# Kernel optimization log

Measured on AMD Instinct MI355X. Metric: run time of the kernel, lower is better.

## Reference

```python
import jax, jax.numpy as jnp
import numpy as np

H = 768            # hidden_size
IMG_H = 1024       # image_hidden_size
NH = 12            # num_heads
NKV = 1            # num_kv_heads (MQA)
HD = H // NH       # head_dim = 64
FF = 4 * H         # intermediate_size = 3072
EPS = 1e-5


def layernorm(x, g, b):
    m = jnp.mean(x, axis=-1, keepdims=True)
    v = jnp.mean(jnp.square(x - m), axis=-1, keepdims=True)
    return (x - m) * jax.lax.rsqrt(v + EPS) * g + b


def setup_inputs() -> dict:
    key = jax.random.key(0)
    ks = jax.random.split(key, 12)
    B, NQ, NIMG = 8, 256, 4096
    s = 0.02
    return {
        "hidden_states": jax.random.normal(ks[0], (B, NQ, H), jnp.float32),
        "image_features": jax.random.normal(ks[1], (B, NIMG, IMG_H), jnp.float32),
        # norm_image_pre
        "ln_img_g": jnp.ones((IMG_H,), jnp.float32),
        "ln_img_b": jnp.zeros((IMG_H,), jnp.float32),
        # image_bottleneck (bias=False)
        "W_bottle": jax.random.normal(ks[2], (IMG_H, H), jnp.float32) * s,
        # norm_hidden
        "ln_h_g": jnp.ones((H,), jnp.float32),
        "ln_h_b": jnp.zeros((H,), jnp.float32),
        # to_q
        "Wq": jax.random.normal(ks[3], (H, H), jnp.float32) * s,
        "bq": jnp.zeros((H,), jnp.float32),
        # to_kv: out = num_kv_heads * head_dim * 2
        "Wkv": jax.random.normal(ks[4], (H, 2 * NKV * HD), jnp.float32) * s,
        "bkv": jnp.zeros((2 * NKV * HD,), jnp.float32),
        # to_out
        "Wo": jax.random.normal(ks[5], (H, H), jnp.float32) * s,
        "bo": jnp.zeros((H,), jnp.float32),
        # attn_out_norm
        "ln_ao_g": jnp.ones((H,), jnp.float32),
        "ln_ao_b": jnp.zeros((H,), jnp.float32),
        # gate
        "gate_param": jnp.zeros((), jnp.float32),
        # ffn_norm
        "ln_f_g": jnp.ones((H,), jnp.float32),
        "ln_f_b": jnp.zeros((H,), jnp.float32),
        # ffn
        "W1": jax.random.normal(ks[6], (H, FF), jnp.float32) * s,
        "b1": jnp.zeros((FF,), jnp.float32),
        "W2": jax.random.normal(ks[7], (FF, H), jnp.float32) * s,
        "b2": jnp.zeros((H,), jnp.float32),
    }


def reference(hidden_states, image_features, ln_img_g, ln_img_b, W_bottle,
              ln_h_g, ln_h_b, Wq, bq, Wkv, bkv, Wo, bo, ln_ao_g, ln_ao_b,
              gate_param, ln_f_g, ln_f_b, W1, b1, W2, b2):
    B, NQ, _ = hidden_states.shape
    # image pre-norm + bottleneck
    img = layernorm(image_features, ln_img_g, ln_img_b)
    img = img @ W_bottle                                   # [B, Nimg, H]
    # query path
    q_in = layernorm(hidden_states, ln_h_g, ln_h_b)
    q = (q_in @ Wq + bq).reshape(B, NQ, NH, HD).transpose(0, 2, 1, 3)  # b h i d
    # kv path (MQA: single shared KV head)
    kv = (img @ Wkv + bkv).reshape(B, -1, 2, NKV, HD)
    k = kv[:, :, 0, 0, :]                                  # [B, Nimg, HD]
    v = kv[:, :, 1, 0, :]
    scale = 1.0 / np.sqrt(HD)
    # broadcast KV across heads instead of explicit repeat
    scores = jnp.einsum('bhid,bjd->bhij', q * scale, k)    # [B, NH, NQ, Nimg]
    attn = jax.nn.softmax(scores, axis=-1)                 # dropout is identity (eval)
    out = jnp.einsum('bhij,bjd->bhid', attn, v)
    out = out.transpose(0, 2, 1, 3).reshape(B, NQ, H)
    out = out @ Wo + bo
    out = layernorm(out, ln_ao_g, ln_ao_b)
    gate = jax.nn.sigmoid(gate_param)
    h = hidden_states + gate * out
    ffn_in = layernorm(h, ln_f_g, ln_f_b)
    ffn_out = jax.nn.gelu(ffn_in @ W1 + b1, approximate=False) @ W2 + b2
    return h + ffn_out
```

## Files before the change

### kernel.cpp

```cpp
#include <hip/hip_runtime.h>
#include <cstdint>

typedef unsigned short u16;
typedef __bf16 bf16_t;
typedef bf16_t bf16x8 __attribute__((ext_vector_type(8)));
typedef float f32x4 __attribute__((ext_vector_type(4)));

__device__ __forceinline__ float b2f(u16 v) {
  union { uint32_t u; float f; } c; c.u = ((uint32_t)v) << 16; return c.f;
}
__device__ __forceinline__ u16 f2b(float f) {
  union { float f; uint32_t u; } c; c.f = f;
  uint32_t lsb = (c.u >> 16) & 1u;
  return (u16)((c.u + 0x7fffu + lsb) >> 16);
}
__device__ __forceinline__ uint4 pack8(f32x4 a, f32x4 b) {
  union { uint4 v; u16 s[8]; } r;
  r.s[0] = f2b(a[0]); r.s[1] = f2b(a[1]); r.s[2] = f2b(a[2]); r.s[3] = f2b(a[3]);
  r.s[4] = f2b(b[0]); r.s[5] = f2b(b[1]); r.s[6] = f2b(b[2]); r.s[7] = f2b(b[3]);
  return r.v;
}
__device__ __forceinline__ uint32_t cvt_pk_bf16(float lo, float hi) {
  uint32_t r;
  asm("v_cvt_pk_bf16_f32 %0, %1, %2" : "=v"(r) : "v"(lo), "v"(hi));
  return r;
}
__device__ __forceinline__ void phase_barrier() {
  asm volatile("s_waitcnt lgkmcnt(0)" ::: "memory");
  __builtin_amdgcn_s_barrier();
  asm volatile("" ::: "memory");
}
__device__ __forceinline__ void vm_drain() {
  asm volatile("s_waitcnt vmcnt(0)" ::: "memory");
}
__device__ __forceinline__ void gload_lds16(const u16* g, u16* l) {
  __builtin_amdgcn_global_load_lds((const __attribute__((address_space(1))) void*)g,
                                   (__attribute__((address_space(3))) void*)l, 16, 0, 0);
}
__device__ __forceinline__ int xcd_swizzle(int lid, int nwg) {
  int q = nwg >> 3, r = nwg & 7, x = lid & 7, s = lid >> 3;
  return (x < r ? x * (q + 1) : r * (q + 1) + (x - r) * q) + s;
}

__global__ __launch_bounds__(256) void transpose_f2b(const float* __restrict__ in,
                                                     u16* __restrict__ out, int R, int C) {
  __shared__ __align__(16) u16 tile[32][33];
  int tx = threadIdx.x & 31, ty = threadIdx.x >> 5;
  int c0 = blockIdx.x * 32, r0 = blockIdx.y * 32;
#pragma unroll
  for (int i = 0; i < 4; ++i) {
    int r = r0 + ty + i * 8, c = c0 + tx;
    if (r < R && c < C) tile[ty + i * 8][tx] = f2b(in[(size_t)r * C + c]);
  }
  __syncthreads();
#pragma unroll
  for (int i = 0; i < 4; ++i) {
    int oc = c0 + ty + i * 8, orr = r0 + tx;
    if (oc < C && orr < R) out[(size_t)oc * R + orr] = tile[tx][ty + i * 8];
  }
}

__global__ __launch_bounds__(256) void prep_wg(const u16* __restrict__ WT, const float* __restrict__ g,
                                               const float* __restrict__ b, u16* __restrict__ WgT,
                                               float* __restrict__ ucol, float* __restrict__ wcol,
                                               int K) {
  int n = blockIdx.x * 4 + (threadIdx.x >> 6);
  int lane = threadIdx.x & 63;
  const u16* src = WT + (size_t)n * K;
  u16* dst = WgT + (size_t)n * K;
  float su = 0.f, sw = 0.f;
  for (int k = lane; k < K; k += 64) {
    float wc = b2f(src[k]);
    float wg = g[k] * wc;
    dst[k] = f2b(wg);
    su += wg;
    sw += b[k] * wc;
  }
#pragma unroll
  for (int off = 32; off >= 1; off >>= 1) {
    su += __shfl_xor(su, off, 64);
    sw += __shfl_xor(sw, off, 64);
  }
  if (lane == 0) { ucol[n] = su; wcol[n] = sw; }
}

__global__ __launch_bounds__(256) void hs_prep(const float* __restrict__ hs, u16* __restrict__ out,
                                               float* __restrict__ rstdg, float* __restrict__ mrstdg) {
  int row = blockIdx.x * 4 + (threadIdx.x >> 6);
  int lane = threadIdx.x & 63;
  const float* x = hs + (size_t)row * 768;
  float v[12];
#pragma unroll
  for (int it = 0; it < 3; ++it) {
    int c = (lane + it * 64) * 4;
    f32x4 d = *(const f32x4*)(x + c);
    v[it * 4 + 0] = d[0]; v[it * 4 + 1] = d[1]; v[it * 4 + 2] = d[2]; v[it * 4 + 3] = d[3];
  }
  float s = 0.f, s2 = 0.f;
#pragma unroll
  for (int i = 0; i < 12; ++i) { s += v[i]; s2 += v[i] * v[i]; }
#pragma unroll
  for (int off = 32; off >= 1; off >>= 1) {
    s += __shfl_xor(s, off, 64);
    s2 += __shfl_xor(s2, off, 64);
  }
  float inv_n = 1.0f / 768.f;
  float mean = s * inv_n;
  float var = fmaxf(s2 * inv_n - mean * mean, 0.f);
  float rstd = rsqrtf(var + 1e-5f);
  if (lane == 0) { rstdg[row] = rstd; mrstdg[row] = mean * rstd; }
#pragma unroll
  for (int it = 0; it < 3; ++it) {
    int c = (lane + it * 64) * 4;
    uint2 po;
    po.x = (uint32_t)f2b(v[it * 4 + 0]) | ((uint32_t)f2b(v[it * 4 + 1]) << 16);
    po.y = (uint32_t)f2b(v[it * 4 + 2]) | ((uint32_t)f2b(v[it * 4 + 3]) << 16);
    *(uint2*)(out + (size_t)row * 768 + c) = po;
  }
}

__global__ __launch_bounds__(256) void ln_res(const u16* __restrict__ ao, const float* __restrict__ g,
                                              const float* __restrict__ bta,
                                              const float* __restrict__ hs,
                                              const float* __restrict__ gatep,
                                              float* __restrict__ hf, u16* __restrict__ hb,
                                              float* __restrict__ rstdg, float* __restrict__ mrstdg) {
  int row = blockIdx.x * 4 + (threadIdx.x >> 6);
  int lane = threadIdx.x & 63;
  const u16* xb = ao + (size_t)row * 768;
  float v[12];
#pragma unroll
  for (int it = 0; it < 3; ++it) {
    int c = (lane + it * 64) * 4;
    uint2 d = *(const uint2*)(xb + c);
    v[it * 4 + 0] = b2f(d.x & 0xffff); v[it * 4 + 1] = b2f(d.x >> 16);
    v[it * 4 + 2] = b2f(d.y & 0xffff); v[it * 4 + 3] = b2f(d.y >> 16);
  }
  float s = 0.f, s2 = 0.f;
#pragma unroll
  for (int i = 0; i < 12; ++i) { s += v[i]; s2 += v[i] * v[i]; }
#pragma unroll
  for (int off = 32; off >= 1; off >>= 1) {
    s += __shfl_xor(s, off, 64);
    s2 += __shfl_xor(s2, off, 64);
  }
  float inv_n = 1.0f / 768.f;
  float mean = s * inv_n;
  float var = fmaxf(s2 * inv_n - mean * mean, 0.f);
  float rstd = rsqrtf(var + 1e-5f);
  float gate = 1.f / (1.f + __expf(-gatep[0]));
  float hsum = 0.f, hsum2 = 0.f;
  float o[12];
#pragma unroll
  for (int it = 0; it < 3; ++it) {
    int c = (lane + it * 64) * 4;
    const float* rr = hs + (size_t)row * 768 + c;
#pragma unroll
    for (int i = 0; i < 4; ++i) {
      float hv = rr[i] + gate * ((v[it * 4 + i] - mean) * rstd * g[c + i] + bta[c + i]);
      o[it * 4 + i] = hv;
      hsum += hv; hsum2 += hv * hv;
    }
    *(f32x4*)(hf + (size_t)row * 768 + c) = (f32x4){o[it * 4 + 0], o[it * 4 + 1], o[it * 4 + 2], o[it * 4 + 3]};
    uint2 po;
    po.x = (uint32_t)f2b(o[it * 4 + 0]) | ((uint32_t)f2b(o[it * 4 + 1]) << 16);
    po.y = (uint32_t)f2b(o[it * 4 + 2]) | ((uint32_t)f2b(o[it * 4 + 3]) << 16);
    *(uint2*)(hb + (size_t)row * 768 + c) = po;
  }
#pragma unroll
  for (int off = 32; off >= 1; off >>= 1) {
    hsum += __shfl_xor(hsum, off, 64);
    hsum2 += __shfl_xor(hsum2, off, 64);
  }
  float hm = hsum * inv_n;
  float hvar = fmaxf(hsum2 * inv_n - hm * hm, 0.f);
  float hrstd = rsqrtf(hvar + 1e-5f);
  if (lane == 0) { rstdg[row] = hrstd; mrstdg[row] = hm * hrstd; }
}

template <int BM, int SPLITK, int AMODE, int BMODE, int EPI, bool OUTF32, bool VTOUT>
__device__ __forceinline__ void gemm_body(const void* __restrict__ Av, const void* __restrict__ Bv,
                                          const float* __restrict__ bias,
                                          const float* __restrict__ rstdg,
                                          const float* __restrict__ mrstdg,
                                          const float* __restrict__ ucol,
                                          const float* __restrict__ wcol,
                                          void* __restrict__ Cv, u16* __restrict__ VTout,
                                          int M, int N, int K) {
  constexpr int MT = BM / 32;
  constexpr int AL = BM / 64;
  __shared__ __align__(16) u16 aT[2][BM * 32];
  __shared__ __align__(16) u16 bT[2][128 * 32];
  __shared__ float rstd_s[EPI == 4 ? 128 : 1];
  __shared__ float mrstd_s[EPI == 4 ? 128 : 1];
  __shared__ __align__(16) u16 vtile[VTOUT ? 64 * 136 : 1];

  int gx = gridDim.x, gy = gridDim.y;
  int nwg = gx * gy * (int)gridDim.z;
  int lid = ((int)blockIdx.z * gy + (int)blockIdx.y) * gx + (int)blockIdx.x;
  int wid = xcd_swizzle(lid, nwg);
  int bz = wid / (gx * gy);
  int rem = wid - bz * (gx * gy);
  int bx = rem / gy;
  int by = rem - bx * gy;

  int t = threadIdx.x, lane = t & 63, wave = t >> 6;
  int quad = lane >> 4, lcol = lane & 15;
  int wm = (wave >> 1) * (16 * MT), wn = (wave & 1) * 64;
  const u16* Ab = (const u16*)Av;
  const float* Af = (const float*)Av;
  const u16* Bb = (const u16*)Bv;
  const float* Bf = (const float*)Bv;
  const int kchunk = (SPLITK > 1) ? K / SPLITK : K;
  const int kstart = (SPLITK > 1) ? bz * kchunk : 0;
  int rr = t >> 1, rc = t & 1;
  float sa = 0.f, sa2 = 0.f;
  f32x4 acc[MT][4];
#pragma unroll
  for (int i = 0; i < MT; ++i)
#pragma unroll
    for (int j = 0; j < 4; ++j) acc[i][j] = (f32x4){0.f, 0.f, 0.f, 0.f};

  f32x4 araw[4], braw[4];

  auto dmaA = [&](int buf, int k0) {
#pragma unroll
    for (int s2 = 0; s2 < AL; ++s2) {
      int row = (wave * AL + s2) * 16 + (lane >> 2);
      int ch = (lane & 3) ^ (row & 3);
      gload_lds16(Ab + (size_t)(bx * BM + row) * K + kstart + k0 + ch * 8,
                  &aT[buf][(wave * AL + s2) * 512]);
    }
  };
  auto dmaB = [&](int buf, int k0) {
#pragma unroll
    for (int s2 = 0; s2 < 2; ++s2) {
      int row = (wave * 2 + s2) * 16 + (lane >> 2);
      int ch = (lane & 3) ^ (row & 3);
      gload_lds16(Bb + (size_t)(by * 128 + row) * K + kstart + k0 + ch * 8,
                  &bT[buf][(wave * 2 + s2) * 512]);
    }
  };
  auto regloadA = [&](int k0) {
    const f32x4* p = (const f32x4*)&Af[(size_t)(bx * BM + rr) * K + kstart + k0 + rc * 16];
#pragma unroll
    for (int i = 0; i < 4; ++i) araw[i] = p[i];
  };
  auto regstoreA = [&](int buf) {
    if (EPI == 4) {
#pragma unroll
      for (int i = 0; i < 4; ++i)
#pragma unroll
        for (int j = 0; j < 4; ++j) { sa += araw[i][j]; sa2 += araw[i][j] * araw[i][j]; }
    }
    uint4 c0 = pack8(araw[0], araw[1]), c1 = pack8(araw[2], araw[3]);
    *(uint4*)&aT[buf][rr * 32 + (((rc * 2 + 0) ^ (rr & 3)) << 3)] = c0;
    *(uint4*)&aT[buf][rr * 32 + (((rc * 2 + 1) ^ (rr & 3)) << 3)] = c1;
  };
  auto regloadB = [&](int k0) {
    const f32x4* p = (const f32x4*)&Bf[(size_t)(by * 128 + rr) * K + kstart + k0 + rc * 16];
#pragma unroll
    for (int i = 0; i < 4; ++i) braw[i] = p[i];
  };
  auto regstoreB = [&](int buf) {
    uint4 c0 = pack8(braw[0], braw[1]), c1 = pack8(braw[2], braw[3]);
    *(uint4*)&bT[buf][rr * 32 + (((rc * 2 + 0) ^ (rr & 3)) << 3)] = c0;
    *(uint4*)&bT[buf][rr * 32 + (((rc * 2 + 1) ^ (rr & 3)) << 3)] = c1;
  };
  auto stage_load = [&](int buf, int k0) {
    if (AMODE == 1) regloadA(k0); else dmaA(buf, k0);
    if (BMODE == 1) regloadB(k0); else dmaB(buf, k0);
  };
  auto stage_store = [&](int buf) {
    if (AMODE == 1) regstoreA(buf);
    if (BMODE == 1) regstoreB(buf);
  };
  auto compute = [&](int buf) {
    bf16x8 af[MT], bfr[4];
#pragma unroll
    for (int mt = 0; mt < MT; ++mt) {
      int r = wm + mt * 16 + lcol;
      af[mt] = *(const bf16x8*)&aT[buf][r * 32 + (((quad ^ (r & 3))) << 3)];
    }
#pragma unroll
    for (int nt = 0; nt < 4; ++nt) {
      int r = wn + nt * 16 + lcol;
      bfr[nt] = *(const bf16x8*)&bT[buf][r * 32 + (((quad ^ (r & 3))) << 3)];
    }
#pragma unroll
    for (int mt = 0; mt < MT; ++mt)
#pragma unroll
      for (int nt = 0; nt < 4; ++nt)
        acc[mt][nt] = __builtin_amdgcn_mfma_f32_16x16x32_bf16(af[mt], bfr[nt], acc[mt][nt], 0, 0, 0);
  };

  const int nk = kchunk >> 5;
  stage_load(0, 0);
  stage_store(0);
  vm_drain();
  phase_barrier();
  int cur = 0;
  for (int kt = 0; kt < nk; ++kt) {
    bool more = kt + 1 < nk;
    if (more) stage_load(cur ^ 1, (kt + 1) << 5);
    compute(cur);
    if (more) stage_store(cur ^ 1);
    vm_drain();
    phase_barrier();
    cur ^= 1;
  }

  if (EPI == 4) {
    float s = sa, s2 = sa2;
    s += __shfl_xor(s, 1, 64);
    s2 += __shfl_xor(s2, 1, 64);
    if ((t & 1) == 0) {
      float inv_n = 1.0f / (float)K;
      float mean = s * inv_n;
      float var = fmaxf(s2 * inv_n - mean * mean, 0.f);
      float rstd = rsqrtf(var + 1e-5f);
      rstd_s[rr] = rstd;
      mrstd_s[rr] = mean * rstd;
    }
    __syncthreads();
  }

  if (VTOUT) {
    u16* kb = (u16*)Cv;
#pragma unroll
    for (int mt = 0; mt < MT; ++mt) {
#pragma unroll
      for (int nt = 0; nt < 4; ++nt) {
#pragma unroll
        for (int r = 0; r < 4; ++r) {
          int lrow = wm + mt * 16 + quad * 4 + r;
          int row = bx * BM + lrow;
          int col = wn + nt * 16 + lcol;
          float v = rstd_s[lrow] * acc[mt][nt][r] - mrstd_s[lrow] * ucol[col] + wcol[col] + bias[col];
          u16 hv = f2b(v);
          if (wn == 0) kb[(size_t)row * 64 + col] = hv;
          else vtile[(col - 64) * 136 + lrow] = hv;
        }
      }
    }
    __syncthreads();
    int dd = t >> 2, js = (t & 3) * 32;
    int bg = bx >> 5, j0g = (bx & 31) * 128;
    u16* dst = VTout + ((size_t)bg * 64 + dd) * 4096 + j0g + js;
#pragma unroll
    for (int i = 0; i < 4; ++i)
      *(uint4*)(dst + i * 8) = *(const uint4*)&vtile[dd * 136 + js + i * 8];
    return;
  }

  u16* Cb = (u16*)Cv;
  float* Cf = (float*)Cv;
  if (SPLITK > 1) Cf += (size_t)bz * (size_t)M * (size_t)N;
#pragma unroll
  for (int mt = 0; mt < MT; ++mt) {
#pragma unroll
    for (int nt = 0; nt < 4; ++nt) {
#pragma unroll
      for (int r = 0; r < 4; ++r) {
        int lrow = wm + mt * 16 + quad * 4 + r;
        int row = bx * BM + lrow;
        int col = by * 128 + wn + nt * 16 + lcol;
        float v = acc[mt][nt][r];
        if (EPI == 1) v += bias[col];
        if (EPI == 3 || EPI == 5)
          v = rstdg[row] * v - mrstdg[row] * ucol[col] + wcol[col] + bias[col];
        if (EPI == 5) v = 0.5f * v * (1.f + erff(v * 0.70710678118f));
        size_t idx = (size_t)row * N + col;
        if (OUTF32) Cf[idx] = v; else Cb[idx] = f2b(v);
      }
    }
  }
}

#define GEMM_ARGS const void* Av, const void* Bv, const float* bias, const float* rstdg, \
                  const float* mrstdg, const float* ucol, const float* wcol, void* Cv,   \
                  u16* VTout, int M, int N, int K
__global__ __launch_bounds__(256) void gemm_wc(GEMM_ARGS) {
  gemm_body<128, 1, 0, 1, 0, false, false>(Av, Bv, bias, rstdg, mrstdg, ucol, wcol, Cv, VTout, M, N, K);
}
__global__ __launch_bounds__(256) void gemm_kv(GEMM_ARGS) {
  gemm_body<128, 1, 1, 0, 4, false, true>(Av, Bv, bias, rstdg, mrstdg, ucol, wcol, Cv, VTout, M, N, K);
}
__global__ __launch_bounds__(256) void gemm_q(GEMM_ARGS) {
  gemm_body<64, 1, 0, 0, 3, false, false>(Av, Bv, bias, rstdg, mrstdg, ucol, wcol, Cv, VTout, M, N, K);
}
__global__ __launch_bounds__(256) void gemm_o(GEMM_ARGS) {
  gemm_body<64, 1, 0, 0, 1, false, false>(Av, Bv, bias, rstdg, mrstdg, ucol, wcol, Cv, VTout, M, N, K);
}
__global__ __launch_bounds__(256) void gemm_w1(GEMM_ARGS) {
  gemm_body<128, 1, 0, 0, 5, false, false>(Av, Bv, bias, rstdg, mrstdg, ucol, wcol, Cv, VTout, M, N, K);
}
__global__ __launch_bounds__(256) void gemm_w2(GEMM_ARGS) {
  gemm_body<64, 2, 0, 0, 0, true, false>(Av, Bv, bias, rstdg, mrstdg, ucol, wcol, Cv, VTout, M, N, K);
}

__global__ __launch_bounds__(256) void w2_merge(const float* __restrict__ part,
                                                const float* __restrict__ hf,
                                                const float* __restrict__ b2,
                                                float* __restrict__ out) {
  int idx = blockIdx.x * 256 + threadIdx.x;
  f32x4 p0 = ((const f32x4*)part)[idx];
  f32x4 p1 = ((const f32x4*)part)[idx + 393216];
  f32x4 h = ((const f32x4*)hf)[idx];
  f32x4 bb = ((const f32x4*)b2)[idx % 192];
  f32x4 o;
#pragma unroll
  for (int i = 0; i < 4; ++i) o[i] = p0[i] + p1[i] + h[i] + bb[i];
  ((f32x4*)out)[idx] = o;
}

__global__ __launch_bounds__(256) void attn_kernel(const u16* __restrict__ qbuf,
                                                   const u16* __restrict__ kb,
                                                   const u16* __restrict__ VT,
                                                   float* __restrict__ Opart,
                                                   float* __restrict__ lpart) {
  __shared__ __align__(16) u16 k_lds[2][64 * 72];
  __shared__ __align__(16) u16 vt_lds[2][64 * 72];
  __shared__ __align__(16) u16 p_lds[4 * 16 * 72];
  int lid = ((int)blockIdx.z * 12 + (int)blockIdx.y) * 4 + (int)blockIdx.x;
  int wid = (lid & 7) * 96 + (lid >> 3);
  int bi = wid & 3;
  int h = (wid >> 2) % 12;
  int z = wid / 48;
  int b = z >> 1, s = z & 1;
  int t = threadIdx.x;
  int wave = t >> 6, lane = t & 63, quad = lane >> 4, lcol = lane & 15;
  int i0 = bi * 64 + wave * 16;
  const u16* qrow = qbuf + ((size_t)(b * 256 + i0 + lcol) * 768 + h * 64 + quad * 8);
  bf16x8 qf0 = *(const bf16x8*)qrow;
  bf16x8 qf1 = *(const bf16x8*)(qrow + 32);
  float l_r[4] = {0.f, 0.f, 0.f, 0.f};
  f32x4 oacc[4];
#pragma unroll
  for (int nt = 0; nt < 4; ++nt) oacc[nt] = (f32x4){0.f, 0.f, 0.f, 0.f};
  int sr = t >> 2, sc = (t & 3) * 16;
  const u16* kbase = kb + (size_t)b * 4096 * 64;
  const u16* vtbase = VT + (size_t)b * 64 * 4096;
  u16* pw = &p_lds[wave * 16 * 72];

  uint4 kr0, kr1, vr0, vr1;
  auto stage_load = [&](int jt) {
    int j0 = s * 2048 + jt * 64;
    const u16* krow = kbase + (size_t)(j0 + sr) * 64 + sc;
    kr0 = *(const uint4*)(krow);
    kr1 = *(const uint4*)(krow + 8);
    const u16* vrow = vtbase + (size_t)sr * 4096 + j0 + sc;
    vr0 = *(const uint4*)(vrow);
    vr1 = *(const uint4*)(vrow + 8);
  };
  auto stage_store = [&](int buf) {
    *(uint4*)&k_lds[buf][sr * 72 + sc] = kr0;
    *(uint4*)&k_lds[buf][sr * 72 + sc + 8] = kr1;
    *(uint4*)&vt_lds[buf][sr * 72 + sc] = vr0;
    *(uint4*)&vt_lds[buf][sr * 72 + sc + 8] = vr1;
  };

  stage_load(0);
  stage_store(0);
  phase_barrier();
  int cur = 0;
  for (int jt = 0; jt < 32; ++jt) {
    bool more = jt + 1 < 32;
    if (more) stage_load(jt + 1);

    f32x4 sc4[4];
#pragma unroll
    for (int nt = 0; nt < 4; ++nt) sc4[nt] = (f32x4){0.f, 0.f, 0.f, 0.f};
    __builtin_amdgcn_s_setprio(1);
#pragma unroll
    for (int nt = 0; nt < 4; ++nt) {
      bf16x8 kb0 = *(const bf16x8*)&k_lds[cur][(nt * 16 + lcol) * 72 + quad * 8];
      bf16x8 kb1 = *(const bf16x8*)&k_lds[cur][(nt * 16 + lcol) * 72 + 32 + quad * 8];
      sc4[nt] = __builtin_amdgcn_mfma_f32_16x16x32_bf16(qf0, kb0, sc4[nt], 0, 0, 0);
      sc4[nt] = __builtin_amdgcn_mfma_f32_16x16x32_bf16(qf1, kb1, sc4[nt], 0, 0, 0);
    }
    __builtin_amdgcn_s_setprio(0);
#pragma unroll
    for (int r = 0; r < 4; ++r) {
      float rsum = 0.f;
#pragma unroll
      for (int nt = 0; nt < 4; ++nt) {
        float p = __expf(sc4[nt][r] * 0.125f);
        sc4[nt][r] = p;
        rsum += p;
      }
      rsum += __shfl_xor(rsum, 1, 64);
      rsum += __shfl_xor(rsum, 2, 64);
      rsum += __shfl_xor(rsum, 4, 64);
      rsum += __shfl_xor(rsum, 8, 64);
      l_r[r] += rsum;
      uint32_t pk01 = cvt_pk_bf16(sc4[0][r], sc4[1][r]);
      uint32_t pk23 = cvt_pk_bf16(sc4[2][r], sc4[3][r]);
      int prow = (quad * 4 + r) * 72 + lcol;
      pw[prow] = (u16)(pk01 & 0xffff);
      pw[prow + 16] = (u16)(pk01 >> 16);
      pw[prow + 32] = (u16)(pk23 & 0xffff);
      pw[prow + 48] = (u16)(pk23 >> 16);
    }
    __builtin_amdgcn_s_setprio(1);
#pragma unroll
    for (int ks = 0; ks < 2; ++ks) {
      bf16x8 pa = *(const bf16x8*)&pw[lcol * 72 + ks * 32 + quad * 8];
#pragma unroll
      for (int nt = 0; nt < 4; ++nt) {
        bf16x8 vb = *(const bf16x8*)&vt_lds[cur][(nt * 16 + lcol) * 72 + ks * 32 + quad * 8];
        oacc[nt] = __builtin_amdgcn_mfma_f32_16x16x32_bf16(pa, vb, oacc[nt], 0, 0, 0);
      }
    }
    __builtin_amdgcn_s_setprio(0);
    if (more) stage_store(cur ^ 1);
    phase_barrier();
    cur ^= 1;
  }
  size_t base = ((size_t)z * 12 + h) * 256;
#pragma unroll
  for (int r = 0; r < 4; ++r) {
    int row = bi * 64 + wave * 16 + quad * 4 + r;
#pragma unroll
    for (int nt = 0; nt < 4; ++nt)
      Opart[(base + row) * 64 + nt * 16 + lcol] = oacc[nt][r];
    if (lcol == 0) lpart[base + row] = l_r[r];
  }
}

__global__ __launch_bounds__(256) void attn_merge(const float* __restrict__ Opart,
                                                  const float* __restrict__ lpart,
                                                  u16* __restrict__ attn_o) {
  int row = blockIdx.x;
  int col = blockIdx.y * 256 + threadIdx.x;
  int b = row >> 8, i = row & 255, h = col >> 6, d = col & 63;
  size_t i0 = (((size_t)(b * 2 + 0) * 12 + h) * 256 + i);
  size_t i1 = (((size_t)(b * 2 + 1) * 12 + h) * 256 + i);
  float o = Opart[i0 * 64 + d] + Opart[i1 * 64 + d];
  float l = lpart[i0] + lpart[i1];
  attn_o[(size_t)row * 768 + col] = f2b(o / l);
}

extern "C" void kernel_launch(void* const* d_in, const int* in_sizes, int n_in, void* d_out,
                              int out_size, void* d_ws, size_t ws_size, hipStream_t stream) {
  (void)in_sizes; (void)n_in; (void)out_size; (void)ws_size;
  const float* hs = (const float*)d_in[0];
  const float* imgf = (const float*)d_in[1];
  const float* ln_img_g = (const float*)d_in[2];
  const float* ln_img_b = (const float*)d_in[3];
  const float* W_bottle = (const float*)d_in[4];
  const float* ln_h_g = (const float*)d_in[5];
  const float* ln_h_b = (const float*)d_in[6];
  const float* Wq = (const float*)d_in[7];
  const float* bq = (const float*)d_in[8];
  const float* Wkv = (const float*)d_in[9];
  const float* bkv = (const float*)d_in[10];
  const float* Wo = (const float*)d_in[11];
  const float* bo = (const float*)d_in[12];
  const float* ln_ao_g = (const float*)d_in[13];
  const float* ln_ao_b = (const float*)d_in[14];
  const float* gatep = (const float*)d_in[15];
  const float* ln_f_g = (const float*)d_in[16];
  const float* ln_f_b = (const float*)d_in[17];
  const float* W1 = (const float*)d_in[18];
  const float* b1 = (const float*)d_in[19];
  const float* W2 = (const float*)d_in[20];
  const float* b2 = (const float*)d_in[21];

  char* sc = (char*)d_ws;
  auto alloc = [&](size_t bytes) {
    char* p = sc;
    sc += (bytes + 63) & ~(size_t)63;
    return p;
  };
  u16* WTq = (u16*)alloc(768 * 768 * 2);
  u16* WTo = (u16*)alloc(768 * 768 * 2);
  u16* WT1 = (u16*)alloc(3072 * 768 * 2);
  u16* WT2 = (u16*)alloc(768 * 3072 * 2);
  u16* WkvT = (u16*)alloc(128 * 768 * 2);
  u16* WcT = (u16*)alloc(128 * 1024 * 2);
  u16* WgT = (u16*)alloc(128 * 1024 * 2);
  u16* WqgT = (u16*)alloc(768 * 768 * 2);
  u16* W1gT = (u16*)alloc(3072 * 768 * 2);
  float* ucol = (float*)alloc(128 * 4);
  float* wcol = (float*)alloc(128 * 4);
  float* uq = (float*)alloc(768 * 4);
  float* wq = (float*)alloc(768 * 4);
  float* u1 = (float*)alloc(3072 * 4);
  float* w1c = (float*)alloc(3072 * 4);
  float* rstdq = (float*)alloc(2048 * 4);
  float* mrstdq = (float*)alloc(2048 * 4);
  float* rstdh = (float*)alloc(2048 * 4);
  float* mrstdh = (float*)alloc(2048 * 4);
  u16* hs16 = (u16*)alloc(2048 * 768 * 2);
  u16* kb = (u16*)alloc((size_t)32768 * 64 * 2);
  u16* VT = (u16*)alloc((size_t)8 * 64 * 4096 * 2);
  u16* qb = (u16*)alloc(2048 * 768 * 2);
  u16* attn_o = (u16*)alloc(2048 * 768 * 2);
  u16* ao = (u16*)alloc(2048 * 768 * 2);
  u16* hbuf = (u16*)alloc(2048 * 768 * 2);
  float* hf32 = (float*)alloc(2048 * 768 * 4);
  u16* actb = (u16*)alloc((size_t)2048 * 3072 * 2);
  float* Opart = (float*)alloc((size_t)16 * 12 * 256 * 64 * 4);
  float* lpart = (float*)alloc((size_t)16 * 12 * 256 * 4);

  transpose_f2b<<<dim3(24, 24), 256, 0, stream>>>(Wq, WTq, 768, 768);
  transpose_f2b<<<dim3(24, 24), 256, 0, stream>>>(Wo, WTo, 768, 768);
  transpose_f2b<<<dim3(96, 24), 256, 0, stream>>>(W1, WT1, 768, 3072);
  transpose_f2b<<<dim3(24, 96), 256, 0, stream>>>(W2, WT2, 3072, 768);
  transpose_f2b<<<dim3(4, 24), 256, 0, stream>>>(Wkv, WkvT, 768, 128);

  gemm_wc<<<dim3(1, 8), 256, 0, stream>>>(WkvT, W_bottle, nullptr, nullptr, nullptr, nullptr,
                                          nullptr, WcT, nullptr, 128, 1024, 768);
  prep_wg<<<32, 256, 0, stream>>>(WcT, ln_img_g, ln_img_b, WgT, ucol, wcol, 1024);
  prep_wg<<<192, 256, 0, stream>>>(WTq, ln_h_g, ln_h_b, WqgT, uq, wq, 768);
  prep_wg<<<768, 256, 0, stream>>>(WT1, ln_f_g, ln_f_b, W1gT, u1, w1c, 768);
  hs_prep<<<512, 256, 0, stream>>>(hs, hs16, rstdq, mrstdq);
  gemm_kv<<<dim3(256, 1), 256, 0, stream>>>(imgf, WgT, bkv, nullptr, nullptr, ucol, wcol,
                                            kb, VT, 32768, 128, 1024);
  gemm_q<<<dim3(32, 6), 256, 0, stream>>>(hs16, WqgT, bq, rstdq, mrstdq, uq, wq,
                                          qb, nullptr, 2048, 768, 768);
  attn_kernel<<<dim3(4, 12, 16), 256, 0, stream>>>(qb, kb, VT, Opart, lpart);
  attn_merge<<<dim3(2048, 3), 256, 0, stream>>>(Opart, lpart, attn_o);
  gemm_o<<<dim3(32, 6), 256, 0, stream>>>(attn_o, WTo, bo, nullptr, nullptr, nullptr, nullptr,
                                          ao, nullptr, 2048, 768, 768);
  ln_res<<<512, 256, 0, stream>>>(ao, ln_ao_g, ln_ao_b, hs, gatep, hf32, hbuf, rstdh, mrstdh);
  gemm_w1<<<dim3(16, 24), 256, 0, stream>>>(hbuf, W1gT, b1, rstdh, mrstdh, u1, w1c,
                                            actb, nullptr, 2048, 3072, 768);
  gemm_w2<<<dim3(32, 6, 2), 256, 0, stream>>>(actb, WT2, nullptr, nullptr, nullptr, nullptr, nullptr,
                                              Opart, nullptr, 2048, 768, 3072);
  w2_merge<<<1536, 256, 0, stream>>>(Opart, hf32, b2, (float*)d_out);
}
```

Before: 519.1 us.

## Quad-buffer DMA GEMM pipeline and split attention KV into four chunks

For GEMMs whose A and B tiles both load through global_load_lds DMA, the K loop now uses four LDS buffers with three stages in flight. It waits on partial vmcnt counts instead of draining all loads every iteration. Separately, the attention kernel splits the 4096-long KV sequence into four chunks instead of two, doubling the grid to 1536 blocks. The merge kernel now sums four partials, in exchange for more partial-output traffic and doubled LDS for the pure-DMA GEMMs.

```diff
diff --git a/kernel.cpp b/kernel.cpp
--- a/kernel.cpp
+++ b/kernel.cpp
@@ -32,6 +32,10 @@
 }
 __device__ __forceinline__ void vm_drain() {
   asm volatile("s_waitcnt vmcnt(0)" ::: "memory");
+}
+template <int N>
+__device__ __forceinline__ void vmwait() {
+  asm volatile("s_waitcnt vmcnt(%0)" :: "n"(N) : "memory");
 }
 __device__ __forceinline__ void gload_lds16(const u16* g, u16* l) {
   __builtin_amdgcn_global_load_lds((const __attribute__((address_space(1))) void*)g,
@@ -189,8 +193,11 @@
                                           int M, int N, int K) {
   constexpr int MT = BM / 32;
   constexpr int AL = BM / 64;
-  __shared__ __align__(16) u16 aT[2][BM * 32];
-  __shared__ __align__(16) u16 bT[2][128 * 32];
+  constexpr bool PURE = (AMODE == 0 && BMODE == 0);
+  constexpr int NBUF = PURE ? 4 : 2;
+  constexpr int LPT = AL + 2;
+  __shared__ __align__(16) u16 aT[NBUF][BM * 32];
+  __shared__ __align__(16) u16 bT[NBUF][128 * 32];
   __shared__ float rstd_s[EPI == 4 ? 128 : 1];
   __shared__ float mrstd_s[EPI == 4 ? 128 : 1];
   __shared__ __align__(16) u16 vtile[VTOUT ? 64 * 136 : 1];
@@ -267,14 +274,6 @@
     *(uint4*)&bT[buf][rr * 32 + (((rc * 2 + 0) ^ (rr & 3)) << 3)] = c0;
     *(uint4*)&bT[buf][rr * 32 + (((rc * 2 + 1) ^ (rr & 3)) << 3)] = c1;
   };
-  auto stage_load = [&](int buf, int k0) {
-    if (AMODE == 1) regloadA(k0); else dmaA(buf, k0);
-    if (BMODE == 1) regloadB(k0); else dmaB(buf, k0);
-  };
-  auto stage_store = [&](int buf) {
-    if (AMODE == 1) regstoreA(buf);
-    if (BMODE == 1) regstoreB(buf);
-  };
   auto compute = [&](int buf) {
     bf16x8 af[MT], bfr[4];
 #pragma unroll
@@ -295,19 +294,42 @@
   };
 
   const int nk = kchunk >> 5;
-  stage_load(0, 0);
-  stage_store(0);
-  vm_drain();
-  phase_barrier();
-  int cur = 0;
-  for (int kt = 0; kt < nk; ++kt) {
-    bool more = kt + 1 < nk;
-    if (more) stage_load(cur ^ 1, (kt + 1) << 5);
-    compute(cur);
-    if (more) stage_store(cur ^ 1);
+  if (PURE) {
+    dmaA(0, 0); dmaB(0, 0);
+    if (nk > 1) { dmaA(1, 1 << 5); dmaB(1, 1 << 5); }
+    if (nk > 2) { dmaA(2, 2 << 5); dmaB(2, 2 << 5); }
+    for (int kt = 0; kt < nk; ++kt) {
+      int left = nk - 1 - kt;
+      if (left >= 2) vmwait<2 * LPT>();
+      else if (left == 1) vmwait<LPT>();
+      else vmwait<0>();
+      phase_barrier();
+      if (kt + 3 < nk) { dmaA((kt + 3) & 3, (kt + 3) << 5); dmaB((kt + 3) & 3, (kt + 3) << 5); }
+      compute(kt & 3);
+    }
+  } else {
+    if (AMODE == 1) regloadA(0); else dmaA(0, 0);
+    if (BMODE == 1) regloadB(0); else dmaB(0, 0);
+    if (AMODE == 1) regstoreA(0);
+    if (BMODE == 1) regstoreB(0);
     vm_drain();
     phase_barrier();
-    cur ^= 1;
+    int cur = 0;
+    for (int kt = 0; kt < nk; ++kt) {
+      bool more = kt + 1 < nk;
+      if (more) {
+        if (AMODE == 1) regloadA((kt + 1) << 5); else dmaA(cur ^ 1, (kt + 1) << 5);
+        if (BMODE == 1) regloadB((kt + 1) << 5); else dmaB(cur ^ 1, (kt + 1) << 5);
+      }
+      compute(cur);
+      if (more) {
+        if (AMODE == 1) regstoreA(cur ^ 1);
+        if (BMODE == 1) regstoreB(cur ^ 1);
+      }
+      vm_drain();
+      phase_barrier();
+      cur ^= 1;
+    }
   }
 
   if (EPI == 4) {
@@ -423,11 +445,11 @@
   __shared__ __align__(16) u16 vt_lds[2][64 * 72];
   __shared__ __align__(16) u16 p_lds[4 * 16 * 72];
   int lid = ((int)blockIdx.z * 12 + (int)blockIdx.y) * 4 + (int)blockIdx.x;
-  int wid = (lid & 7) * 96 + (lid >> 3);
+  int wid = (lid & 7) * 192 + (lid >> 3);
   int bi = wid & 3;
   int h = (wid >> 2) % 12;
   int z = wid / 48;
-  int b = z >> 1, s = z & 1;
+  int b = z >> 2, s = z & 3;
   int t = threadIdx.x;
   int wave = t >> 6, lane = t & 63, quad = lane >> 4, lcol = lane & 15;
   int i0 = bi * 64 + wave * 16;
@@ -445,7 +467,7 @@
 
   uint4 kr0, kr1, vr0, vr1;
   auto stage_load = [&](int jt) {
-    int j0 = s * 2048 + jt * 64;
+    int j0 = s * 1024 + jt * 64;
     const u16* krow = kbase + (size_t)(j0 + sr) * 64 + sc;
     kr0 = *(const uint4*)(krow);
     kr1 = *(const uint4*)(krow + 8);
@@ -464,8 +486,8 @@
   stage_store(0);
   phase_barrier();
   int cur = 0;
-  for (int jt = 0; jt < 32; ++jt) {
-    bool more = jt + 1 < 32;
+  for (int jt = 0; jt < 16; ++jt) {
+    bool more = jt + 1 < 16;
     if (more) stage_load(jt + 1);
 
     f32x4 sc4[4];
@@ -534,10 +556,13 @@
   int row = blockIdx.x;
   int col = blockIdx.y * 256 + threadIdx.x;
   int b = row >> 8, i = row & 255, h = col >> 6, d = col & 63;
-  size_t i0 = (((size_t)(b * 2 + 0) * 12 + h) * 256 + i);
-  size_t i1 = (((size_t)(b * 2 + 1) * 12 + h) * 256 + i);
-  float o = Opart[i0 * 64 + d] + Opart[i1 * 64 + d];
-  float l = lpart[i0] + lpart[i1];
+  float o = 0.f, l = 0.f;
+#pragma unroll
+  for (int s = 0; s < 4; ++s) {
+    size_t ii = (((size_t)(b * 4 + s) * 12 + h) * 256 + i);
+    o += Opart[ii * 64 + d];
+    l += lpart[ii];
+  }
   attn_o[(size_t)row * 768 + col] = f2b(o / l);
 }
 
@@ -601,8 +626,8 @@
   u16* hbuf = (u16*)alloc(2048 * 768 * 2);
   float* hf32 = (float*)alloc(2048 * 768 * 4);
   u16* actb = (u16*)alloc((size_t)2048 * 3072 * 2);
-  float* Opart = (float*)alloc((size_t)16 * 12 * 256 * 64 * 4);
-  float* lpart = (float*)alloc((size_t)16 * 12 * 256 * 4);
+  float* Opart = (float*)alloc((size_t)32 * 12 * 256 * 64 * 4);
+  float* lpart = (float*)alloc((size_t)32 * 12 * 256 * 4);
 
   transpose_f2b<<<dim3(24, 24), 256, 0, stream>>>(Wq, WTq, 768, 768);
   transpose_f2b<<<dim3(24, 24), 256, 0, stream>>>(Wo, WTo, 768, 768);
@@ -620,7 +645,7 @@
                                             kb, VT, 32768, 128, 1024);
   gemm_q<<<dim3(32, 6), 256, 0, stream>>>(hs16, WqgT, bq, rstdq, mrstdq, uq, wq,
                                           qb, nullptr, 2048, 768, 768);
-  attn_kernel<<<dim3(4, 12, 16), 256, 0, stream>>>(qb, kb, VT, Opart, lpart);
+  attn_kernel<<<dim3(4, 12, 32), 256, 0, stream>>>(qb, kb, VT, Opart, lpart);
   attn_merge<<<dim3(2048, 3), 256, 0, stream>>>(Opart, lpart, attn_o);
   gemm_o<<<dim3(32, 6), 256, 0, stream>>>(attn_o, WTo, bo, nullptr, nullptr, nullptr, nullptr,
                                           ao, nullptr, 2048, 768, 768);
```

After: 522.3 us. No clear change (+0.6%).
